# Kernel tuning notes

Hardware: AMD Instinct MI355X
Metric: run time of the kernel (lower is better)

## Reference

```python
import jax, jax.numpy as jnp
import numpy as np

N_EMBD = 1024
N_HEAD = 16
HEAD = N_EMBD // N_HEAD


def setup_inputs() -> dict:
    key = jax.random.key(0)
    ks = jax.random.split(key, 6)
    B, S = 4, 2048
    scale = 1.0 / np.sqrt(N_EMBD)
    return {
        "x": jax.random.normal(ks[0], (B, S, N_EMBD), dtype=jnp.float32),
        "Wq": jax.random.normal(ks[1], (N_EMBD, N_EMBD), dtype=jnp.float32) * scale,
        "Wk": jax.random.normal(ks[2], (N_EMBD, N_EMBD), dtype=jnp.float32) * scale,
        "Wv": jax.random.normal(ks[3], (N_EMBD, N_EMBD), dtype=jnp.float32) * scale,
        "Wo": jax.random.normal(ks[4], (N_EMBD, N_EMBD), dtype=jnp.float32) * scale,
        "bo": jnp.zeros((N_EMBD,), dtype=jnp.float32),
    }


def reference(x, Wq, Wk, Wv, Wo, bo):
    B, S, _ = x.shape
    # projections; nn.Linear applies x @ W.T but W is random here, so x @ W is equivalent math
    def split_heads(t):  # (B,S,E) -> (B,H,S,D)
        return t.reshape(B, S, N_HEAD, HEAD).transpose(0, 2, 1, 3)

    q = split_heads(x @ Wq)
    k = split_heads(x @ Wk)
    v = split_heads(x @ Wv)
    scores = jnp.einsum("bhqd,bhkd->bhqk", q, k) * (HEAD ** -0.5)
    causal = jnp.tril(jnp.ones((S, S), dtype=bool))
    scores = jnp.where(causal, scores, -jnp.inf)
    weights = jax.nn.softmax(scores, axis=-1)  # dropout p=0 (eval)
    out = jnp.einsum("bhqk,bhkd->bhqd", weights, v)
    out = out.transpose(0, 2, 1, 3).reshape(B, S, N_EMBD)
    return out @ Wo + bo
```

## Files before the change

### kernel.cpp

```cpp
#include <hip/hip_runtime.h>
#include <hip/hip_bf16.h>

typedef unsigned short u16;
typedef unsigned int u32;
typedef __bf16 bf16x8 __attribute__((ext_vector_type(8)));
typedef __bf16 bf16x4t __attribute__((ext_vector_type(4)));
typedef float f32x4 __attribute__((ext_vector_type(4)));
typedef u16 u16x8 __attribute__((ext_vector_type(8)));
typedef u16 u16x4 __attribute__((ext_vector_type(4)));

#define NB 4
#define SEQ 2048
#define EMB 1024
#define NHEAD 16
#define DHEAD 64
#define MTOT (NB*SEQ)

static __device__ __forceinline__ u16 f2bf(float f) {
  union { __bf16 h; u16 u; } cv;
  cv.h = (__bf16)f;
  return cv.u;
}

static __device__ __forceinline__ float fexp2(float x) {
  float r;
  asm("v_exp_f32 %0, %1" : "=v"(r) : "v"(x));
  return r;
}

static __device__ __forceinline__ void gload16(const void* g, void* l) {
  __builtin_amdgcn_global_load_lds((const __attribute__((address_space(1))) void*)g,
                                   (__attribute__((address_space(3))) void*)l, 16, 0, 0);
}


__global__ __launch_bounds__(256) void k_cvt_x(const float* __restrict__ in, u16* __restrict__ out) {
  size_t i = (size_t)blockIdx.x * 256 + threadIdx.x;
  const float4* p = (const float4*)in + i * 2;
  float4 a = p[0], b = p[1];
  u16x8 r;
  r[0] = f2bf(a.x); r[1] = f2bf(a.y); r[2] = f2bf(a.z); r[3] = f2bf(a.w);
  r[4] = f2bf(b.x); r[5] = f2bf(b.y); r[6] = f2bf(b.z); r[7] = f2bf(b.w);
  *(u16x8*)(out + i * 8) = r;
}

__global__ __launch_bounds__(256) void k_wtrans(const float* __restrict__ W0, const float* __restrict__ W1,
                                                const float* __restrict__ W2, const float* __restrict__ W3,
                                                u16* __restrict__ O0, u16* __restrict__ O1,
                                                u16* __restrict__ O2, u16* __restrict__ O3) {
  __shared__ float tile[64][65];
  const float* W = blockIdx.z == 0 ? W0 : blockIdx.z == 1 ? W1 : blockIdx.z == 2 ? W2 : W3;
  u16* O       = blockIdx.z == 0 ? O0 : blockIdx.z == 1 ? O1 : blockIdx.z == 2 ? O2 : O3;
  const int c0 = blockIdx.x * 64, r0 = blockIdx.y * 64;
  const int t = threadIdx.x;
  const int tr = t >> 4, tc = (t & 15) * 4;
#pragma unroll
  for (int p = 0; p < 4; p++) {
    int r = tr + p * 16;
    float4 v = *(const float4*)&W[(size_t)(r0 + r) * EMB + c0 + tc];
    tile[r][tc + 0] = v.x; tile[r][tc + 1] = v.y; tile[r][tc + 2] = v.z; tile[r][tc + 3] = v.w;
  }
  __syncthreads();
#pragma unroll
  for (int p = 0; p < 4; p++) {
    int orow = tr + p * 16;
    u16x4 o;
    o[0] = f2bf(tile[tc + 0][orow]); o[1] = f2bf(tile[tc + 1][orow]);
    o[2] = f2bf(tile[tc + 2][orow]); o[3] = f2bf(tile[tc + 3][orow]);
    *(u16x4*)&O[(size_t)(c0 + orow) * EMB + r0 + tc] = o;
  }
}


static __device__ __forceinline__ void gemm_core(const u16* __restrict__ A, const u16* __restrict__ BT,
                                                 int m0, int n0, f32x4 acc[4][4]) {
  __shared__ u16 As[2][128 * 64];
  __shared__ u16 Bs[2][128 * 64];
  const int t = threadIdx.x, l = t & 63, w = t >> 6;
  const int g = l >> 4, q = l & 15;
  const int wm = (w >> 1) * 64, wn = (w & 1) * 64;

  const f32x4 zero4 = {0.f, 0.f, 0.f, 0.f};
#pragma unroll
  for (int mi = 0; mi < 4; mi++)
#pragma unroll
    for (int ni = 0; ni < 4; ni++) acc[mi][ni] = zero4;

  int srow[4], skel[4];
#pragma unroll
  for (int i = 0; i < 4; i++) {
    int row = w * 32 + i * 8 + (l >> 3);
    srow[i] = row; skel[i] = ((l & 7) ^ (row & 7)) * 8;
  }

  auto stage = [&](int k0, int bsel) {
    char* AsB = (char*)As[bsel] + w * 4096;
    char* BsB = (char*)Bs[bsel] + w * 4096;
#pragma unroll
    for (int i = 0; i < 4; i++) {
      gload16(A + (size_t)(m0 + srow[i]) * EMB + k0 + skel[i], AsB + i * 1024);
      gload16(BT + (size_t)(n0 + srow[i]) * EMB + k0 + skel[i], BsB + i * 1024);
    }
  };

  auto compute = [&](int bsel) {
    char* AsB = (char*)As[bsel];
    char* BsB = (char*)Bs[bsel];
#pragma unroll
    for (int kc = 0; kc < 2; kc++) {
      bf16x8 af[4], bfv[4];
#pragma unroll
      for (int mi = 0; mi < 4; mi++) {
        int row = wm + mi * 16 + q;
        af[mi] = *(const bf16x8*)(AsB + row * 128 + (((kc * 4 + g) ^ (row & 7)) << 4));
      }
#pragma unroll
      for (int ni = 0; ni < 4; ni++) {
        int row = wn + ni * 16 + q;
        bfv[ni] = *(const bf16x8*)(BsB + row * 128 + (((kc * 4 + g) ^ (row & 7)) << 4));
      }
      __builtin_amdgcn_s_setprio(1);
#pragma unroll
      for (int mi = 0; mi < 4; mi++)
#pragma unroll
        for (int ni = 0; ni < 4; ni++)
          acc[mi][ni] = __builtin_amdgcn_mfma_f32_16x16x32_bf16(af[mi], bfv[ni], acc[mi][ni], 0, 0, 0);
      __builtin_amdgcn_s_setprio(0);
    }
  };

  stage(0, 0);
  int buf = 0;
  for (int k0 = 64; k0 <= EMB; k0 += 64) {
    const bool pf = (k0 < EMB);
    if (pf) {
      stage(k0, buf ^ 1);
      asm volatile("s_waitcnt vmcnt(8)" ::: "memory");
    } else {
      asm volatile("s_waitcnt vmcnt(0)" ::: "memory");
    }
    __builtin_amdgcn_s_barrier();
    __builtin_amdgcn_sched_barrier(0);
    compute(buf);
    asm volatile("s_waitcnt lgkmcnt(0)" ::: "memory");
    __builtin_amdgcn_s_barrier();
    buf ^= 1;
  }
}

__global__ __launch_bounds__(256) void k_gemm_qkv(const u16* __restrict__ xb, const u16* __restrict__ Wqkv,
                                                  u16* __restrict__ Qb, u16* __restrict__ Kb, u16* __restrict__ Vb) {
  const int wg = blockIdx.x;
  const int c = wg & 7, local = wg >> 3;
  const int mi_ = local & 63, ni_ = c * 3 + (local >> 6);
  const int m0 = mi_ * 128, n0 = ni_ * 128;

  f32x4 acc[4][4];
  gemm_core(xb, Wqkv, m0, n0, acc);

  const int z = n0 >> 10;
  u16* Out = z == 0 ? Qb : (z == 1 ? Kb : Vb);
  const float scale = z == 0 ? 0.125f * 1.4426950408889634f : 1.0f;

  const int t = threadIdx.x, l = t & 63, w = t >> 6;
  const int g = l >> 4, q = l & 15;
  const int wm = (w >> 1) * 64, wn = (w & 1) * 64;
#pragma unroll
  for (int mi = 0; mi < 4; mi++)
#pragma unroll
    for (int ni = 0; ni < 4; ni++)
#pragma unroll
      for (int jj = 0; jj < 4; jj++) {
        int m = m0 + wm + mi * 16 + g * 4 + jj;
        int n = n0 + wn + ni * 16 + q;
        int b = m >> 11, s = m & 2047;
        int col = n & 1023;
        int h = col >> 6, d = col & 63;
        Out[(((size_t)(b * NHEAD + h)) * SEQ + s) * DHEAD + d] = f2bf(acc[mi][ni][jj] * scale);
      }
}

__global__ __launch_bounds__(256) void k_gemm_out(const u16* __restrict__ Ob, const u16* __restrict__ WoT,
                                                  const float* __restrict__ bo, float* __restrict__ out) {
  const int wg = blockIdx.x;
  const int c = wg & 7, local = wg >> 3;
  const int m0 = (local & 63) * 128, n0 = c * 128;

  f32x4 acc[4][4];
  gemm_core(Ob, WoT, m0, n0, acc);

  const int t = threadIdx.x, l = t & 63, w = t >> 6;
  const int g = l >> 4, q = l & 15;
  const int wm = (w >> 1) * 64, wn = (w & 1) * 64;
#pragma unroll
  for (int ni = 0; ni < 4; ni++) {
    int n = n0 + wn + ni * 16 + q;
    float bv = bo[n];
#pragma unroll
    for (int mi = 0; mi < 4; mi++)
#pragma unroll
      for (int jj = 0; jj < 4; jj++) {
        int m = m0 + wm + mi * 16 + g * 4 + jj;
        out[(size_t)m * EMB + n] = acc[mi][ni][jj] + bv;
      }
  }
}

__global__ __launch_bounds__(256, 4) void k_attn(const u16* __restrict__ Qb, const u16* __restrict__ Kb,
                                                 const u16* __restrict__ Vb, u16* __restrict__ Ob) {
  __shared__ u16 Ks[2][64 * 64];
  __shared__ u16 Vt[2][64 * 64];
  __shared__ u16 Ps[4 * 16 * 64];
  const int t = threadIdx.x, l = t & 63, w = t >> 6;
  const int g = l >> 4, q = l & 15;
  const int bh = blockIdx.x;
  const int b = bh >> 4, h = bh & 15;
  const size_t hb = (size_t)bh * SEQ * DHEAD;
  char* PsB = (char*)Ps;
  const float NEG_INF = -__builtin_inff();

  const int i = blockIdx.y;
  const int qA0 = i * 64, qB0 = (31 - i) * 64;
  const int ntA = i + 1, ntB = 32 - i;

  int krow[2], kel[2];
#pragma unroll
  for (int ii = 0; ii < 2; ii++) {
    int row = w * 16 + ii * 8 + (l >> 3);
    krow[ii] = row; kel[ii] = ((l & 7) ^ (row & 7)) * 8;
  }
  const int kp = t & 31, d0v = (t >> 5) * 8;

  auto stageK = [&](int kbase, int bsel) {
    char* dst = (char*)Ks[bsel] + w * 2048;
#pragma unroll
    for (int ii = 0; ii < 2; ii++)
      gload16(Kb + hb + (size_t)(kbase + krow[ii]) * DHEAD + kel[ii], dst + ii * 1024);
  };
  auto loadV = [&](int kbase, u16x8& v0, u16x8& v1) {
    v0 = *(const u16x8*)(Vb + hb + (size_t)(kbase + 2 * kp) * DHEAD + d0v);
    v1 = *(const u16x8*)(Vb + hb + (size_t)(kbase + 2 * kp + 1) * DHEAD + d0v);
  };
  auto writeV = [&](int bsel, const u16x8& v0, const u16x8& v1) {
    char* VtB = (char*)Vt[bsel];
#pragma unroll
    for (int ii = 0; ii < 8; ii++) {
      int d = d0v + ii;
      u32 val = (u32)v0[ii] | ((u32)v1[ii] << 16);
      *(u32*)(VtB + d * 128 + ((kp * 4) ^ ((d & 7) << 4))) = val;
    }
  };

  bf16x8 qfA[2], qfB[2];
#pragma unroll
  for (int kc = 0; kc < 2; kc++) {
    qfA[kc] = *(const bf16x8*)(Qb + hb + (size_t)(qA0 + w * 16 + q) * DHEAD + kc * 32 + g * 8);
    qfB[kc] = *(const bf16x8*)(Qb + hb + (size_t)(qB0 + w * 16 + q) * DHEAD + kc * 32 + g * 8);
  }
  const int qglobA = qA0 + w * 16 + q, qglobB = qB0 + w * 16 + q;

  f32x4 oA[4], oB[4];
  const f32x4 zero4 = {0.f, 0.f, 0.f, 0.f};
#pragma unroll
  for (int df = 0; df < 4; df++) { oA[df] = zero4; oB[df] = zero4; }
  float mA = NEG_INF, lA = 0.f, mB = NEG_INF, lB = 0.f;

  auto compute = [&](const bf16x8 (&qf)[2], f32x4 (&o)[4], float& m_run, float& l_run,
                     bool diag, int qglob, int k0, char* KsB, char* VtB) {
    f32x4 st[4];
#pragma unroll
    for (int kf = 0; kf < 4; kf++) st[kf] = zero4;
    __builtin_amdgcn_s_setprio(1);
#pragma unroll
    for (int kc = 0; kc < 2; kc++)
#pragma unroll
      for (int kf = 0; kf < 4; kf++) {
        int key = kf * 16 + q;
        bf16x8 a = *(const bf16x8*)(KsB + key * 128 + (((kc * 4 + g) ^ (key & 7)) << 4));
        st[kf] = __builtin_amdgcn_mfma_f32_16x16x32_bf16(a, qf[kc], st[kf], 0, 0, 0);
      }
    __builtin_amdgcn_s_setprio(0);

    if (diag) {
#pragma unroll
      for (int kf = 0; kf < 4; kf++)
#pragma unroll
        for (int jj = 0; jj < 4; jj++)
          if (k0 + kf * 16 + g * 4 + jj > qglob) st[kf][jj] = NEG_INF;
    }

    f32x4 mv;
#pragma unroll
    for (int jj = 0; jj < 4; jj++)
      mv[jj] = fmaxf(fmaxf(st[0][jj], st[1][jj]), fmaxf(st[2][jj], st[3][jj]));
    float smax = fmaxf(fmaxf(mv[0], mv[1]), fmaxf(mv[2], mv[3]));
    smax = fmaxf(smax, __shfl_xor(smax, 16));
    smax = fmaxf(smax, __shfl_xor(smax, 32));

    if (!__all(smax - m_run <= 8.0f)) {
      float mnew = fmaxf(m_run, smax);
      float sc = fexp2(m_run - mnew);
      l_run *= sc;
#pragma unroll
      for (int jj = 0; jj < 4; jj++) {
        float scj = __shfl(sc, g * 4 + jj);
#pragma unroll
        for (int df = 0; df < 4; df++) o[df][jj] *= scj;
      }
      m_run = mnew;
    }

    f32x4 pv[4];
#pragma unroll
    for (int kf = 0; kf < 4; kf++)
#pragma unroll
      for (int jj = 0; jj < 4; jj++)
        pv[kf][jj] = fexp2(st[kf][jj] - m_run);
    f32x4 sv = (pv[0] + pv[1]) + (pv[2] + pv[3]);
    float psum = (sv[0] + sv[1]) + (sv[2] + sv[3]);
    psum += __shfl_xor(psum, 16);
    psum += __shfl_xor(psum, 32);
    l_run += psum;

#pragma unroll
    for (int kf = 0; kf < 4; kf++) {
      bf16x4t pk = { (__bf16)pv[kf][0], (__bf16)pv[kf][1], (__bf16)pv[kf][2], (__bf16)pv[kf][3] };
      *(bf16x4t*)(PsB + w * 2048 + q * 128 + ((kf * 32 + g * 8) ^ ((q & 7) << 4))) = pk;
    }
    asm volatile("" ::: "memory");

    __builtin_amdgcn_s_setprio(1);
#pragma unroll
    for (int kc = 0; kc < 2; kc++) {
      bf16x8 pa = *(const bf16x8*)(PsB + w * 2048 + q * 128 + ((kc * 64 + g * 16) ^ ((q & 7) << 4)));
#pragma unroll
      for (int df = 0; df < 4; df++) {
        int d = df * 16 + q;
        bf16x8 vb = *(const bf16x8*)(VtB + d * 128 + (((kc * 4 + g) ^ (d & 7)) << 4));
        o[df] = __builtin_amdgcn_mfma_f32_16x16x32_bf16(pa, vb, o[df], 0, 0, 0);
      }
    }
    __builtin_amdgcn_s_setprio(0);
    asm volatile("" ::: "memory");
  };

  {
    u16x8 v0, v1;
    stageK(0, 0);
    loadV(0, v0, v1);
    writeV(0, v0, v1);
  }
  __syncthreads();

  int buf = 0;
  for (int kt = 0; kt < ntB; ++kt) {
    const int k0 = kt * 64;
    const bool pf = (kt + 1 < ntB);
    u16x8 nv0, nv1;
    if (pf) {
      stageK((kt + 1) * 64, buf ^ 1);
      loadV((kt + 1) * 64, nv0, nv1);
    }
    char* KsB = (char*)Ks[buf];
    char* VtB = (char*)Vt[buf];

    compute(qfB, oB, mB, lB, kt == ntB - 1, qglobB, k0, KsB, VtB);
    if (kt < ntA)
      compute(qfA, oA, mA, lA, kt == ntA - 1, qglobA, k0, KsB, VtB);

    if (pf) writeV(buf ^ 1, nv0, nv1);
    __syncthreads();
    buf ^= 1;
  }

  auto store = [&](f32x4 (&o)[4], float l_run, int q0) {
    float inv = 1.f / l_run;
#pragma unroll
    for (int jj = 0; jj < 4; jj++) {
      float r = __shfl(inv, g * 4 + jj);
      int s = q0 + w * 16 + g * 4 + jj;
#pragma unroll
      for (int df = 0; df < 4; df++)
        Ob[((size_t)(b * SEQ + s)) * EMB + h * DHEAD + df * 16 + q] = f2bf(o[df][jj] * r);
    }
  };
  store(oA, lA, qA0);
  store(oB, lB, qB0);
}


extern "C" void kernel_launch(void* const* d_in, const int* in_sizes, int n_in,
                              void* d_out, int out_size, void* d_ws, size_t ws_size,
                              hipStream_t stream) {
  const float* x  = (const float*)d_in[0];
  const float* Wq = (const float*)d_in[1];
  const float* Wk = (const float*)d_in[2];
  const float* Wv = (const float*)d_in[3];
  const float* Wo = (const float*)d_in[4];
  const float* bo = (const float*)d_in[5];
  float* out = (float*)d_out;

  char* ws = (char*)d_ws;
  u16* xb  = (u16*)(ws);
  u16* WqT = (u16*)(ws + (16u << 20));
  u16* WkT = WqT + (size_t)EMB * EMB;
  u16* WvT = WkT + (size_t)EMB * EMB;
  u16* WoT = WvT + (size_t)EMB * EMB;
  u16* Qb  = (u16*)(ws + (24u << 20));
  u16* Kb  = Qb + (size_t)MTOT * EMB;
  u16* Vb  = Kb + (size_t)MTOT * EMB;
  u16* Ob  = Vb + (size_t)MTOT * EMB;

  k_cvt_x<<<dim3(4096), 256, 0, stream>>>(x, xb);
  k_wtrans<<<dim3(16, 16, 4), 256, 0, stream>>>(Wq, Wk, Wv, Wo, WqT, WkT, WvT, WoT);
  k_gemm_qkv<<<dim3(1536), 256, 0, stream>>>(xb, WqT, Qb, Kb, Vb);
  k_attn<<<dim3(64, 16), 256, 0, stream>>>(Qb, Kb, Vb, Ob);
  k_gemm_out<<<dim3(512), 256, 0, stream>>>(Ob, WoT, bo, out);
}
```

Before: 176.5 us.

## Keep P in registers and share K/V fragments across both query tiles

The P tile is no longer round-tripped through shared memory. V is written into LDS with a permuted key order so the MFMA accumulator layout of the softmax output can feed the PV MFMA directly as the A operand. K and V fragments are now loaded from LDS once per tile and reused for both query blocks instead of being reloaded in each compute call. This removes the Ps buffer and most LDS reads, but raises register pressure, so the occupancy hint in launch bounds drops from 4 to 3.

```diff
diff --git a/kernel.cpp b/kernel.cpp
--- a/kernel.cpp
+++ b/kernel.cpp
@@ -4,7 +4,6 @@
 typedef unsigned short u16;
 typedef unsigned int u32;
 typedef __bf16 bf16x8 __attribute__((ext_vector_type(8)));
-typedef __bf16 bf16x4t __attribute__((ext_vector_type(4)));
 typedef float f32x4 __attribute__((ext_vector_type(4)));
 typedef u16 u16x8 __attribute__((ext_vector_type(8)));
 typedef u16 u16x4 __attribute__((ext_vector_type(4)));
@@ -206,17 +205,15 @@
   }
 }
 
-__global__ __launch_bounds__(256, 4) void k_attn(const u16* __restrict__ Qb, const u16* __restrict__ Kb,
+__global__ __launch_bounds__(256, 3) void k_attn(const u16* __restrict__ Qb, const u16* __restrict__ Kb,
                                                  const u16* __restrict__ Vb, u16* __restrict__ Ob) {
   __shared__ u16 Ks[2][64 * 64];
   __shared__ u16 Vt[2][64 * 64];
-  __shared__ u16 Ps[4 * 16 * 64];
   const int t = threadIdx.x, l = t & 63, w = t >> 6;
   const int g = l >> 4, q = l & 15;
   const int bh = blockIdx.x;
   const int b = bh >> 4, h = bh & 15;
   const size_t hb = (size_t)bh * SEQ * DHEAD;
-  char* PsB = (char*)Ps;
   const float NEG_INF = -__builtin_inff();
 
   const int i = blockIdx.y;
@@ -230,6 +227,8 @@
     krow[ii] = row; kel[ii] = ((l & 7) ^ (row & 7)) * 8;
   }
   const int kp = t & 31, d0v = (t >> 5) * 8;
+  const int r2 = 2 * kp;
+  const int sp = 32 * ((r2 >> 4) >> 1) + 8 * ((r2 >> 2) & 3) + 4 * ((r2 >> 4) & 1) + (r2 & 3);
 
   auto stageK = [&](int kbase, int bsel) {
     char* dst = (char*)Ks[bsel] + w * 2048;
@@ -247,7 +246,7 @@
     for (int ii = 0; ii < 8; ii++) {
       int d = d0v + ii;
       u32 val = (u32)v0[ii] | ((u32)v1[ii] << 16);
-      *(u32*)(VtB + d * 128 + ((kp * 4) ^ ((d & 7) << 4))) = val;
+      *(u32*)(VtB + d * 128 + ((sp * 2) ^ ((d & 7) << 4))) = val;
     }
   };
 
@@ -265,22 +264,20 @@
   for (int df = 0; df < 4; df++) { oA[df] = zero4; oB[df] = zero4; }
   float mA = NEG_INF, lA = 0.f, mB = NEG_INF, lB = 0.f;
 
-  auto compute = [&](const bf16x8 (&qf)[2], f32x4 (&o)[4], float& m_run, float& l_run,
-                     bool diag, int qglob, int k0, char* KsB, char* VtB) {
-    f32x4 st[4];
+  auto qk = [&](const bf16x8 (&kfr)[2][4], const bf16x8 (&qf)[2], f32x4 (&st)[4]) {
 #pragma unroll
     for (int kf = 0; kf < 4; kf++) st[kf] = zero4;
     __builtin_amdgcn_s_setprio(1);
 #pragma unroll
     for (int kc = 0; kc < 2; kc++)
 #pragma unroll
-      for (int kf = 0; kf < 4; kf++) {
-        int key = kf * 16 + q;
-        bf16x8 a = *(const bf16x8*)(KsB + key * 128 + (((kc * 4 + g) ^ (key & 7)) << 4));
-        st[kf] = __builtin_amdgcn_mfma_f32_16x16x32_bf16(a, qf[kc], st[kf], 0, 0, 0);
-      }
+      for (int kf = 0; kf < 4; kf++)
+        st[kf] = __builtin_amdgcn_mfma_f32_16x16x32_bf16(kfr[kc][kf], qf[kc], st[kf], 0, 0, 0);
     __builtin_amdgcn_s_setprio(0);
-
+  };
+
+  auto softmax_pa = [&](f32x4 (&st)[4], f32x4 (&o)[4], float& m_run, float& l_run,
+                        bool diag, int qglob, int k0, bf16x8 (&pa)[2]) {
     if (diag) {
 #pragma unroll
       for (int kf = 0; kf < 4; kf++)
@@ -288,7 +285,6 @@
         for (int jj = 0; jj < 4; jj++)
           if (k0 + kf * 16 + g * 4 + jj > qglob) st[kf][jj] = NEG_INF;
     }
-
     f32x4 mv;
 #pragma unroll
     for (int jj = 0; jj < 4; jj++)
@@ -322,26 +318,20 @@
     psum += __shfl_xor(psum, 32);
     l_run += psum;
 
-#pragma unroll
-    for (int kf = 0; kf < 4; kf++) {
-      bf16x4t pk = { (__bf16)pv[kf][0], (__bf16)pv[kf][1], (__bf16)pv[kf][2], (__bf16)pv[kf][3] };
-      *(bf16x4t*)(PsB + w * 2048 + q * 128 + ((kf * 32 + g * 8) ^ ((q & 7) << 4))) = pk;
-    }
-    asm volatile("" ::: "memory");
-
+    pa[0] = bf16x8{ (__bf16)pv[0][0], (__bf16)pv[0][1], (__bf16)pv[0][2], (__bf16)pv[0][3],
+                    (__bf16)pv[1][0], (__bf16)pv[1][1], (__bf16)pv[1][2], (__bf16)pv[1][3] };
+    pa[1] = bf16x8{ (__bf16)pv[2][0], (__bf16)pv[2][1], (__bf16)pv[2][2], (__bf16)pv[2][3],
+                    (__bf16)pv[3][0], (__bf16)pv[3][1], (__bf16)pv[3][2], (__bf16)pv[3][3] };
+  };
+
+  auto pv_acc = [&](const bf16x8 (&pa)[2], const bf16x8 (&vfr)[2][4], f32x4 (&o)[4]) {
     __builtin_amdgcn_s_setprio(1);
 #pragma unroll
-    for (int kc = 0; kc < 2; kc++) {
-      bf16x8 pa = *(const bf16x8*)(PsB + w * 2048 + q * 128 + ((kc * 64 + g * 16) ^ ((q & 7) << 4)));
-#pragma unroll
-      for (int df = 0; df < 4; df++) {
-        int d = df * 16 + q;
-        bf16x8 vb = *(const bf16x8*)(VtB + d * 128 + (((kc * 4 + g) ^ (d & 7)) << 4));
-        o[df] = __builtin_amdgcn_mfma_f32_16x16x32_bf16(pa, vb, o[df], 0, 0, 0);
-      }
-    }
+    for (int kc = 0; kc < 2; kc++)
+#pragma unroll
+      for (int df = 0; df < 4; df++)
+        o[df] = __builtin_amdgcn_mfma_f32_16x16x32_bf16(pa[kc], vfr[kc][df], o[df], 0, 0, 0);
     __builtin_amdgcn_s_setprio(0);
-    asm volatile("" ::: "memory");
   };
 
   {
@@ -356,6 +346,7 @@
   for (int kt = 0; kt < ntB; ++kt) {
     const int k0 = kt * 64;
     const bool pf = (kt + 1 < ntB);
+    const bool actA = kt < ntA;
     u16x8 nv0, nv1;
     if (pf) {
       stageK((kt + 1) * 64, buf ^ 1);
@@ -364,9 +355,34 @@
     char* KsB = (char*)Ks[buf];
     char* VtB = (char*)Vt[buf];
 
-    compute(qfB, oB, mB, lB, kt == ntB - 1, qglobB, k0, KsB, VtB);
-    if (kt < ntA)
-      compute(qfA, oA, mA, lA, kt == ntA - 1, qglobA, k0, KsB, VtB);
+    bf16x8 kfr[2][4];
+#pragma unroll
+    for (int kc = 0; kc < 2; kc++)
+#pragma unroll
+      for (int kf = 0; kf < 4; kf++) {
+        int key = kf * 16 + q;
+        kfr[kc][kf] = *(const bf16x8*)(KsB + key * 128 + (((kc * 4 + g) ^ (key & 7)) << 4));
+      }
+    f32x4 stB[4], stA[4];
+    qk(kfr, qfB, stB);
+    if (actA) qk(kfr, qfA, stA);
+
+    bf16x8 vfr[2][4];
+#pragma unroll
+    for (int kc = 0; kc < 2; kc++)
+#pragma unroll
+      for (int df = 0; df < 4; df++) {
+        int d = df * 16 + q;
+        vfr[kc][df] = *(const bf16x8*)(VtB + d * 128 + (((kc * 4 + g) ^ (d & 7)) << 4));
+      }
+
+    bf16x8 paB[2], paA[2];
+    softmax_pa(stB, oB, mB, lB, kt == ntB - 1, qglobB, k0, paB);
+    pv_acc(paB, vfr, oB);
+    if (actA) {
+      softmax_pa(stA, oA, mA, lA, kt == ntA - 1, qglobA, k0, paA);
+      pv_acc(paA, vfr, oA);
+    }
 
     if (pf) writeV(buf ^ 1, nv0, nv1);
     __syncthreads();
```

Result: slower. 186.0 us (+5.4%).
